# Performance work log

Measured on AMD Instinct MI355X. Metric: run time of the kernel, lower is better.

## Reference

```python
import jax, jax.numpy as jnp
import numpy as np

N, D, H, DH, FF, NE, NNZ = 4096, 128, 2, 64, 256, 2048, 65536
EPS = 1e-5

def layer_norm(x, g, b):
    m = jnp.mean(x, axis=-1, keepdims=True)
    v = jnp.var(x, axis=-1, keepdims=True)
    return (x - m) / jnp.sqrt(v + EPS) * g + b

def setup_inputs() -> dict:
    key = jax.random.key(0)
    ks = jax.random.split(key, 24)
    s = 0.05
    node_idx = jax.random.randint(ks[1], (NNZ,), 0, N)
    he_idx = jax.random.randint(ks[2], (NNZ,), 0, NE)
    return {
        "x": jax.random.normal(ks[0], (N, D), dtype=jnp.float32),
        "edge": jnp.stack([node_idx, he_idx]).astype(jnp.int64),
        "Wq": jax.random.normal(ks[3], (D, D)) * s, "bq": jnp.zeros((D,)),
        "Wk": jax.random.normal(ks[4], (D, D)) * s, "bk": jnp.zeros((D,)),
        "Wv": jax.random.normal(ks[5], (D, D)) * s, "bv": jnp.zeros((D,)),
        "Wo": jax.random.normal(ks[6], (D, D)) * s, "bo": jnp.zeros((D,)),
        "g_ln1": jnp.ones((D,)), "b_ln1": jnp.zeros((D,)),
        "W1": jax.random.normal(ks[7], (D, FF)) * s, "bf1": jnp.zeros((FF,)),
        "W2": jax.random.normal(ks[8], (FF, D)) * s, "bf2": jnp.zeros((D,)),
        "g_ln2": jnp.ones((D,)), "b_ln2": jnp.zeros((D,)),
        "Wh": jax.random.normal(ks[9], (D, D)) * s, "bh": jnp.zeros((D,)),
    }

def reference(x, edge, Wq, bq, Wk, bk, Wv, bv, Wo, bo, g_ln1, b_ln1,
              W1, bf1, W2, bf2, g_ln2, b_ln2, Wh, bh):
    # dropout layers run in eval mode (identity) for a deterministic reference
    def mha_block(h):
        q = (h @ Wq + bq).reshape(N, H, DH)
        k = (h @ Wk + bk).reshape(N, H, DH)
        v = (h @ Wv + bv).reshape(N, H, DH)
        scores = jnp.einsum('nhd,mhd->hnm', q, k) / jnp.sqrt(jnp.float32(DH))
        attn = jax.nn.softmax(scores, axis=-1)            # [H,N,N]
        o = jnp.einsum('hnm,mhd->nhd', attn, v).reshape(N, D)
        return layer_norm(h + o @ Wo + bo, g_ln1, b_ln1)

    def ff_block(h):
        z = jax.nn.sigmoid(h @ W1 + bf1)
        return layer_norm(h + z @ W2 + bf2, g_ln2, b_ln2)

    h = ff_block(mha_block(x))
    h = ff_block(mha_block(h))

    # HypergraphConv: out = D^{-1} H B^{-1} H^T (X Theta) + bias
    node_idx = edge[0]
    he_idx = edge[1]
    xt = h @ Wh                                            # [N,D]
    ones = jnp.ones((NNZ,), dtype=xt.dtype)
    Bdeg = jax.ops.segment_sum(ones, he_idx, num_segments=NE)
    Binv = jnp.where(Bdeg > 0, 1.0 / Bdeg, 0.0)
    Ddeg = jax.ops.segment_sum(ones, node_idx, num_segments=N)
    Dinv = jnp.where(Ddeg > 0, 1.0 / Ddeg, 0.0)
    e = jax.ops.segment_sum(xt[node_idx], he_idx, num_segments=NE) * Binv[:, None]
    out = jax.ops.segment_sum(e[he_idx], node_idx, num_segments=N) * Dinv[:, None] + bh
    return jax.nn.relu(out)
```

## Files before the change

### kernel.cpp

```cpp
#include <hip/hip_runtime.h>
#include <hip/hip_bf16.h>
#include <cstddef>

#define N_NODES 4096
#define DIM     128
#define NHEAD   2
#define DHEAD   64
#define FFDIM   256
#define NEDGE   2048
#define NNZ_E   65536
#define NSPLIT  8

typedef __attribute__((ext_vector_type(8))) short bf16x8;
typedef __attribute__((ext_vector_type(4))) float f32x4;
typedef unsigned short u16;

__device__ __forceinline__ u16 f2b(float f) {
    unsigned u = __float_as_uint(f);
    return (u16)((u + 0x7FFFu + ((u >> 16) & 1u)) >> 16);
}
__device__ __forceinline__ float b2f_bits(u16 h) {
    return __uint_as_float(((unsigned)h) << 16);
}
__device__ __forceinline__ unsigned cvtpk(float a, float b) {
    unsigned r;
    asm("v_cvt_pk_bf16_f32 %0, %1, %2" : "=v"(r) : "v"(a), "v"(b));
    return r;
}

__global__ void prep(const float* __restrict__ x, float* __restrict__ h,
                     u16* __restrict__ hh, u16* __restrict__ hl,
                     const float* W0, const float* W1, const float* W2,
                     const float* W3, const float* W4, const float* W5,
                     const float* W6,
                     u16* P0, u16* P1, u16* P2, u16* P3, u16* P4, u16* P5, u16* P6,
                     const int* __restrict__ edge_raw,
                     int* __restrict__ nidx, int* __restrict__ hidx,
                     int* __restrict__ cnt_e, int* __restrict__ cnt_n) {
    const int bx = blockIdx.x;
    if (bx < 2048) {
        int i = bx * 256 + threadIdx.x;
        float f = x[i];
        h[i] = f;
        u16 hi = f2b(f);
        hh[i] = hi;
        hl[i] = f2b(f - b2f_bits(hi));
        return;
    }
    if (bx >= 2944) {
        __shared__ int is64_s;
        if (threadIdx.x < 64) {
            int v = edge_raw[2 * threadIdx.x + 1];
            unsigned long long bal = __ballot(v != 0);
            if (threadIdx.x == 0) is64_s = (bal == 0ull) ? 1 : 0;
        }
        __syncthreads();
        const int is64 = is64_s;
        int i = (bx - 2944) * 256 + threadIdx.x;
        if (i < NNZ_E) {
            int ni = (is64 ? edge_raw[2 * i]             : edge_raw[i])         & (N_NODES - 1);
            int he = (is64 ? edge_raw[2 * NNZ_E + 2 * i] : edge_raw[NNZ_E + i]) & (NEDGE - 1);
            nidx[i] = ni;
            hidx[i] = he;
            atomicAdd(&cnt_n[ni], 1);
            atomicAdd(&cnt_e[he], 1);
        }
        return;
    }
    const int p = bx - 2048;
    const int sel = p >> 7;
    const float* W; u16* P; int K, NC;
    switch (sel) {
        case 0: W = W0; P = P0; K = 128; NC = 128; break;
        case 1: W = W1; P = P1; K = 128; NC = 128; break;
        case 2: W = W2; P = P2; K = 128; NC = 128; break;
        case 3: W = W3; P = P3; K = 128; NC = 128; break;
        case 4: W = W4; P = P4; K = 128; NC = 128; break;
        case 5: W = W5; P = P5; K = 128; NC = 256; break;
        default: W = W6; P = P6; K = 256; NC = 128; break;
    }
    int i = (p & 127) * 256 + threadIdx.x;
    if (i < K * NC) {
        int k = i / NC, n = i % NC;
        float f = W[i];
        u16 hb = f2b(f);
        size_t o = ((size_t)(k >> 3) * NC + n) * 8 + (k & 7);
        P[o] = hb;
        P[(size_t)K * NC + o] = f2b(f - b2f_bits(hb));
    }
}

__global__ __launch_bounds__(256) void qkv_mfma(const u16* __restrict__ Ah,
                                                const u16* __restrict__ Al,
                                                const u16* __restrict__ Wq,
                                                const u16* __restrict__ Wk,
                                                const u16* __restrict__ Wv,
                                                const float* __restrict__ bq,
                                                const float* __restrict__ bk,
                                                const float* __restrict__ bv,
                                                u16* __restrict__ qb,
                                                u16* __restrict__ kb,
                                                u16* __restrict__ vtb) {
    const int K = 128, NC = 128;
    const int tid = threadIdx.x, w = tid >> 6, lane = tid & 63;
    const int qi = lane & 15, gi = lane >> 4;
    const int row0 = blockIdx.x * 64 + w * 16;
    const int sel = blockIdx.y >> 2;
    const int col0 = (blockIdx.y & 3) * 32;
    const u16* Wp = (sel == 0) ? Wq : (sel == 1) ? Wk : Wv;
    const float* bias = (sel == 0) ? bq : (sel == 1) ? bk : bv;
    const u16* Wlo = Wp + (size_t)K * NC;

    f32x4 acc[2];
    acc[0] = (f32x4){0.f, 0.f, 0.f, 0.f};
    acc[1] = (f32x4){0.f, 0.f, 0.f, 0.f};

#pragma unroll 4
    for (int kc = 0; kc < K / 32; ++kc) {
        const int k0 = kc * 32;
        const size_t ao = (size_t)(row0 + qi) * K + k0 + gi * 8;
        bf16x8 ah = *(const bf16x8*)(Ah + ao);
        bf16x8 al = *(const bf16x8*)(Al + ao);
#pragma unroll
        for (int c = 0; c < 2; ++c) {
            const size_t wo = ((size_t)(k0 / 8 + gi) * NC + col0 + c * 16 + qi) * 8;
            bf16x8 wh = *(const bf16x8*)(Wp + wo);
            bf16x8 wl = *(const bf16x8*)(Wlo + wo);
            acc[c] = __builtin_amdgcn_mfma_f32_16x16x32_bf16(ah, wh, acc[c], 0, 0, 0);
            acc[c] = __builtin_amdgcn_mfma_f32_16x16x32_bf16(al, wh, acc[c], 0, 0, 0);
            acc[c] = __builtin_amdgcn_mfma_f32_16x16x32_bf16(ah, wl, acc[c], 0, 0, 0);
        }
    }

#pragma unroll
    for (int c = 0; c < 2; ++c) {
        const int col = col0 + c * 16 + qi;
        const int hh = col >> 6, d = col & 63;
        float bv_ = bias[col];
        if (sel < 2) {
            u16* dst = (sel == 0) ? qb : kb;
#pragma unroll
            for (int r = 0; r < 4; ++r) {
                const int grow = row0 + gi * 4 + r;
                dst[((size_t)hh * N_NODES + grow) * 64 + d] = f2b(acc[c][r] + bv_);
            }
        } else {
            const int grow0 = row0 + gi * 4;
            uint2 pw;
            pw.x = cvtpk(acc[c][0] + bv_, acc[c][1] + bv_);
            pw.y = cvtpk(acc[c][2] + bv_, acc[c][3] + bv_);
            *(uint2*)&vtb[((size_t)hh * 64 + d) * N_NODES + grow0] = pw;
        }
    }
}

#define ROWP 72
__global__ __launch_bounds__(512) void attn_mfma(const u16* __restrict__ qb,
                                                 const u16* __restrict__ kb,
                                                 const u16* __restrict__ vtb,
                                                 float* __restrict__ op,
                                                 float* __restrict__ mlm,
                                                 float* __restrict__ mll) {
    __shared__ __align__(16) u16 k_s[64 * ROWP];
    __shared__ __align__(16) u16 vt_s[64 * ROWP];
    __shared__ __align__(16) u16 p_s[8][16 * ROWP];
    const int h = blockIdx.y;
    const int s = blockIdx.z;
    const int row0 = blockIdx.x * 128;
    const int tid = threadIdx.x;
    const int w = tid >> 6, lane = tid & 63;
    const int qi = lane & 15, gi = lane >> 4;
    const float CE = 0.18033688011f;
    const float THR = 44.36f;

    const u16* qrow = qb + ((size_t)h * N_NODES + row0 + w * 16 + qi) * 64 + gi * 8;
    bf16x8 qf0 = *(const bf16x8*)qrow;
    bf16x8 qf1 = *(const bf16x8*)(qrow + 32);

    f32x4 oc[4];
#pragma unroll
    for (int i = 0; i < 4; ++i) oc[i] = (f32x4){0.f, 0.f, 0.f, 0.f};
    float m_run = -INFINITY, l_run = 0.f;

    const u16* kbh = kb + (size_t)h * N_NODES * 64;
    const u16* vth = vtb + (size_t)h * 64 * N_NODES;

    for (int kt = s * (N_NODES / 64 / NSPLIT); kt < (s + 1) * (N_NODES / 64 / NSPLIT); ++kt) {
        const u16* ksrc = kbh + kt * 64 * 64;
        {
            int r = tid >> 3, ss = tid & 7;
            *(uint4*)&k_s[r * ROWP + ss * 8]  = *(const uint4*)(ksrc + tid * 8);
            *(uint4*)&vt_s[r * ROWP + ss * 8] = *(const uint4*)(vth + (size_t)r * N_NODES + kt * 64 + ss * 8);
        }
        __syncthreads();

        f32x4 sc[4];
#pragma unroll
        for (int t = 0; t < 4; ++t) {
            const u16* krow = &k_s[(t * 16 + qi) * ROWP + gi * 8];
            bf16x8 ka0 = *(const bf16x8*)krow;
            bf16x8 ka1 = *(const bf16x8*)(krow + 32);
            f32x4 z = (f32x4){0.f, 0.f, 0.f, 0.f};
            z = __builtin_amdgcn_mfma_f32_16x16x32_bf16(ka0, qf0, z, 0, 0, 0);
            sc[t] = __builtin_amdgcn_mfma_f32_16x16x32_bf16(ka1, qf1, z, 0, 0, 0);
        }

        float smax = -INFINITY;
#pragma unroll
        for (int t = 0; t < 4; ++t)
            smax = fmaxf(smax, fmaxf(fmaxf(sc[t][0], sc[t][1]), fmaxf(sc[t][2], sc[t][3])));
        smax = fmaxf(smax, __shfl_xor(smax, 16));
        smax = fmaxf(smax, __shfl_xor(smax, 32));

        const bool renew = !__all(smax <= m_run + THR);
        float alpha;
        if (renew) {
            float mn = fmaxf(m_run, smax);
            alpha = exp2f((m_run - mn) * CE);
            m_run = mn;
        }
        float nb = m_run * CE;
        float psum = 0.f;
#pragma unroll
        for (int t = 0; t < 4; ++t) {
            float p0 = exp2f(fmaf(sc[t][0], CE, -nb));
            float p1 = exp2f(fmaf(sc[t][1], CE, -nb));
            float p2 = exp2f(fmaf(sc[t][2], CE, -nb));
            float p3 = exp2f(fmaf(sc[t][3], CE, -nb));
            psum += (p0 + p1) + (p2 + p3);
            uint2 pw;
            pw.x = cvtpk(p0, p1);
            pw.y = cvtpk(p2, p3);
            *(uint2*)&p_s[w][qi * ROWP + t * 16 + gi * 4] = pw;
        }
        psum += __shfl_xor(psum, 16);
        psum += __shfl_xor(psum, 32);

        if (renew) {
            float a0 = __shfl(alpha, gi * 4 + 0);
            float a1 = __shfl(alpha, gi * 4 + 1);
            float a2 = __shfl(alpha, gi * 4 + 2);
            float a3 = __shfl(alpha, gi * 4 + 3);
#pragma unroll
            for (int d = 0; d < 4; ++d) {
                oc[d][0] *= a0; oc[d][1] *= a1; oc[d][2] *= a2; oc[d][3] *= a3;
            }
            l_run = l_run * alpha + psum;
        } else {
            l_run += psum;
        }

        const u16* prow = &p_s[w][qi * ROWP];
        bf16x8 pa0 = *(const bf16x8*)(prow + gi * 8);
        bf16x8 pa1 = *(const bf16x8*)(prow + 32 + gi * 8);
#pragma unroll
        for (int d = 0; d < 4; ++d) {
            const u16* vrow = &vt_s[(d * 16 + qi) * ROWP + gi * 8];
            bf16x8 vb0 = *(const bf16x8*)vrow;
            bf16x8 vb1 = *(const bf16x8*)(vrow + 32);
            oc[d] = __builtin_amdgcn_mfma_f32_16x16x32_bf16(pa0, vb0, oc[d], 0, 0, 0);
            oc[d] = __builtin_amdgcn_mfma_f32_16x16x32_bf16(pa1, vb1, oc[d], 0, 0, 0);
        }
        __syncthreads();
    }

    float* opd = op + (size_t)s * N_NODES * 128;
#pragma unroll
    for (int d = 0; d < 4; ++d) {
        size_t cb = h * 64 + d * 16 + qi;
        opd[(size_t)(row0 + w * 16 + gi * 4 + 0) * 128 + cb] = oc[d][0];
        opd[(size_t)(row0 + w * 16 + gi * 4 + 1) * 128 + cb] = oc[d][1];
        opd[(size_t)(row0 + w * 16 + gi * 4 + 2) * 128 + cb] = oc[d][2];
        opd[(size_t)(row0 + w * 16 + gi * 4 + 3) * 128 + cb] = oc[d][3];
    }
    if (gi == 0) {
        size_t mi = (size_t)s * NHEAD * N_NODES + (size_t)h * N_NODES + row0 + w * 16 + qi;
        mlm[mi] = m_run;
        mll[mi] = l_run;
    }
}

#define ROWA 136
#define ROWZ 264
#define ROWH 132
template<int DO_QKV>
__global__ __launch_bounds__(512) void mega_layer(
        const float* __restrict__ op, const float* __restrict__ mlm,
        const float* __restrict__ mll,
        const u16* __restrict__ wp_o, const float* __restrict__ bo,
        float* __restrict__ h,
        const float* __restrict__ g1, const float* __restrict__ b1,
        const u16* __restrict__ wp_1, const float* __restrict__ bf1,
        const u16* __restrict__ wp_2, const float* __restrict__ bf2,
        const float* __restrict__ g2, const float* __restrict__ b2,
        const u16* __restrict__ wp_q, const u16* __restrict__ wp_k,
        const u16* __restrict__ wp_v,
        const float* __restrict__ bq, const float* __restrict__ bk,
        const float* __restrict__ bv,
        u16* __restrict__ qb, u16* __restrict__ kb, u16* __restrict__ vtb,
        const u16* __restrict__ wp_h, float* __restrict__ xt) {
    __shared__ __align__(16) u16 zbuf[16 * ROWZ * 2];
    __shared__ __align__(16) u16 hp_hi[16 * ROWA];
    __shared__ __align__(16) u16 hp_lo[16 * ROWA];
    __shared__ float hln[16 * ROWH];
    __shared__ float ws_s[NSPLIT][32];
    __shared__ float Linv_s[32];
    __shared__ float wsum[8][16], wsq[8][16];
    const float CE = 0.18033688011f;
    const int tid = threadIdx.x, w = tid >> 6, lane = tid & 63;
    const int qi = lane & 15, gi = lane >> 4;
    const int row0 = blockIdx.x * 16;
    u16* a_hi = zbuf;
    u16* a_lo = zbuf + 16 * ROWA;
    u16* z_hi = zbuf;
    u16* z_lo = zbuf + 16 * ROWZ;

    if (tid < 32) {
        int r = tid >> 1, hd = tid & 1;
        size_t mb = (size_t)hd * N_NODES + row0 + r;
        float m[NSPLIT], l[NSPLIT], mx = -INFINITY;
#pragma unroll
        for (int s = 0; s < NSPLIT; ++s) {
            m[s] = mlm[mb + (size_t)s * NHEAD * N_NODES];
            l[s] = mll[mb + (size_t)s * NHEAD * N_NODES];
            mx = fmaxf(mx, m[s]);
        }
        float L = 0.f;
#pragma unroll
        for (int s = 0; s < NSPLIT; ++s) {
            float ws = exp2f((m[s] - mx) * CE);
            ws_s[s][tid] = ws;
            L += ws * l[s];
        }
        Linv_s[tid] = 1.f / L;
    }
    __syncthreads();

    for (int e = tid; e < 16 * 128; e += 512) {
        int r = e >> 7, c = e & 127, hd = c >> 6;
        size_t idx = (size_t)(row0 + r) * 128 + c;
        float O = 0.f;
#pragma unroll
        for (int s = 0; s < NSPLIT; ++s)
            O += ws_s[s][r * 2 + hd] * op[(size_t)s * N_NODES * 128 + idx];
        float v = O * Linv_s[r * 2 + hd];
        u16 hi = f2b(v);
        a_hi[r * ROWA + c] = hi;
        a_lo[r * ROWA + c] = f2b(v - b2f_bits(hi));
    }
    __syncthreads();

    {
        const u16* Wlo = wp_o + (size_t)128 * 128;
        f32x4 acc = (f32x4){0.f, 0.f, 0.f, 0.f};
        const int col0 = w * 16;
#pragma unroll
        for (int kc = 0; kc < 4; ++kc) {
            const int k0 = kc * 32;
            bf16x8 ah = *(const bf16x8*)&a_hi[qi * ROWA + k0 + gi * 8];
            bf16x8 al = *(const bf16x8*)&a_lo[qi * ROWA + k0 + gi * 8];
            const size_t wo = ((size_t)(k0 / 8 + gi) * 128 + col0 + qi) * 8;
            bf16x8 wh = *(const bf16x8*)(wp_o + wo);
            bf16x8 wl = *(const bf16x8*)(Wlo + wo);
            acc = __builtin_amdgcn_mfma_f32_16x16x32_bf16(ah, wh, acc, 0, 0, 0);
            acc = __builtin_amdgcn_mfma_f32_16x16x32_bf16(al, wh, acc, 0, 0, 0);
            acc = __builtin_amdgcn_mfma_f32_16x16x32_bf16(ah, wl, acc, 0, 0, 0);
        }
        float y[4], rs[4], rq[4];
        const int col = col0 + qi;
        float bvv = bo[col];
#pragma unroll
        for (int r = 0; r < 4; ++r) {
            float v = acc[r] + bvv + h[(size_t)(row0 + gi * 4 + r) * 128 + col];
            y[r] = v;
            rs[r] = v; rq[r] = v * v;
        }
#pragma unroll
        for (int r = 0; r < 4; ++r)
            for (int msk = 1; msk < 16; msk <<= 1) {
                rs[r] += __shfl_xor(rs[r], msk);
                rq[r] += __shfl_xor(rq[r], msk);
            }
        if (qi == 0) {
#pragma unroll
            for (int r = 0; r < 4; ++r) { wsum[w][gi * 4 + r] = rs[r]; wsq[w][gi * 4 + r] = rq[r]; }
        }
        __syncthreads();
#pragma unroll
        for (int r = 0; r < 4; ++r) {
            const int lr = gi * 4 + r;
            float ts = 0.f, tq = 0.f;
#pragma unroll
            for (int ww = 0; ww < 8; ++ww) { ts += wsum[ww][lr]; tq += wsq[ww][lr]; }
            float mean = ts * (1.f / 128.f);
            float var  = tq * (1.f / 128.f) - mean * mean;
            float rstd = rsqrtf(var + 1e-5f);
            float yn = (y[r] - mean) * rstd * g1[col] + b1[col];
            hln[lr * ROWH + col] = yn;
            u16 hi = f2b(yn);
            hp_hi[lr * ROWA + col] = hi;
            hp_lo[lr * ROWA + col] = f2b(yn - b2f_bits(hi));
        }
    }
    __syncthreads();

    {
        const u16* W1lo = wp_1 + (size_t)128 * 256;
        f32x4 acc1[2];
#pragma unroll
        for (int t = 0; t < 2; ++t) acc1[t] = (f32x4){0.f, 0.f, 0.f, 0.f};
#pragma unroll
        for (int kc = 0; kc < 4; ++kc) {
            const int k0 = kc * 32;
            bf16x8 ah = *(const bf16x8*)&hp_hi[qi * ROWA + k0 + gi * 8];
            bf16x8 al = *(const bf16x8*)&hp_lo[qi * ROWA + k0 + gi * 8];
#pragma unroll
            for (int t = 0; t < 2; ++t) {
                const size_t wo = ((size_t)(k0 / 8 + gi) * 256 + w * 32 + t * 16 + qi) * 8;
                bf16x8 wh = *(const bf16x8*)(wp_1 + wo);
                bf16x8 wl = *(const bf16x8*)(W1lo + wo);
                acc1[t] = __builtin_amdgcn_mfma_f32_16x16x32_bf16(ah, wh, acc1[t], 0, 0, 0);
                acc1[t] = __builtin_amdgcn_mfma_f32_16x16x32_bf16(al, wh, acc1[t], 0, 0, 0);
                acc1[t] = __builtin_amdgcn_mfma_f32_16x16x32_bf16(ah, wl, acc1[t], 0, 0, 0);
            }
        }
        __syncthreads();
#pragma unroll
        for (int t = 0; t < 2; ++t) {
            const int col = w * 32 + t * 16 + qi;
            float bvv = bf1[col];
#pragma unroll
            for (int r = 0; r < 4; ++r) {
                float v = acc1[t][r] + bvv;
                v = 1.f / (1.f + __expf(-v));
                u16 hi = f2b(v);
                const int zr = gi * 4 + r;
                z_hi[zr * ROWZ + col] = hi;
                z_lo[zr * ROWZ + col] = f2b(v - b2f_bits(hi));
            }
        }
    }
    __syncthreads();

    {
        const u16* W2lo = wp_2 + (size_t)256 * 128;
        f32x4 acc = (f32x4){0.f, 0.f, 0.f, 0.f};
        const int col0 = w * 16;
#pragma unroll
        for (int kc = 0; kc < 8; ++kc) {
            const int k0 = kc * 32;
            bf16x8 ah = *(const bf16x8*)&z_hi[qi * ROWZ + k0 + gi * 8];
            bf16x8 al = *(const bf16x8*)&z_lo[qi * ROWZ + k0 + gi * 8];
            const size_t wo = ((size_t)(k0 / 8 + gi) * 128 + col0 + qi) * 8;
            bf16x8 wh = *(const bf16x8*)(wp_2 + wo);
            bf16x8 wl = *(const bf16x8*)(W2lo + wo);
            acc = __builtin_amdgcn_mfma_f32_16x16x32_bf16(ah, wh, acc, 0, 0, 0);
            acc = __builtin_amdgcn_mfma_f32_16x16x32_bf16(al, wh, acc, 0, 0, 0);
            acc = __builtin_amdgcn_mfma_f32_16x16x32_bf16(ah, wl, acc, 0, 0, 0);
        }
        float y[4], rs[4], rq[4];
        const int col = col0 + qi;
        float bvv = bf2[col];
#pragma unroll
        for (int r = 0; r < 4; ++r) {
            float v = acc[r] + bvv + hln[(gi * 4 + r) * ROWH + col];
            y[r] = v;
            rs[r] = v; rq[r] = v * v;
        }
#pragma unroll
        for (int r = 0; r < 4; ++r)
            for (int msk = 1; msk < 16; msk <<= 1) {
                rs[r] += __shfl_xor(rs[r], msk);
                rq[r] += __shfl_xor(rq[r], msk);
            }
        if (qi == 0) {
#pragma unroll
            for (int r = 0; r < 4; ++r) { wsum[w][gi * 4 + r] = rs[r]; wsq[w][gi * 4 + r] = rq[r]; }
        }
        __syncthreads();
#pragma unroll
        for (int r = 0; r < 4; ++r) {
            const int lr = gi * 4 + r;
            float ts = 0.f, tq = 0.f;
#pragma unroll
            for (int ww = 0; ww < 8; ++ww) { ts += wsum[ww][lr]; tq += wsq[ww][lr]; }
            float mean = ts * (1.f / 128.f);
            float var  = tq * (1.f / 128.f) - mean * mean;
            float rstd = rsqrtf(var + 1e-5f);
            float yn = (y[r] - mean) * rstd * g2[col] + b2[col];
            if (DO_QKV) h[(size_t)(row0 + lr) * 128 + col] = yn;
            u16 hi = f2b(yn);
            hp_hi[lr * ROWA + col] = hi;
            hp_lo[lr * ROWA + col] = f2b(yn - b2f_bits(hi));
        }
    }

    if (DO_QKV) {
        __syncthreads();
        const int col0 = w * 16;
#pragma unroll
        for (int sel = 0; sel < 3; ++sel) {
            const u16* Wp = (sel == 0) ? wp_q : (sel == 1) ? wp_k : wp_v;
            const float* bias = (sel == 0) ? bq : (sel == 1) ? bk : bv;
            const u16* Wlo = Wp + (size_t)128 * 128;
            f32x4 acc = (f32x4){0.f, 0.f, 0.f, 0.f};
#pragma unroll
            for (int kc = 0; kc < 4; ++kc) {
                const int k0 = kc * 32;
                bf16x8 ah = *(const bf16x8*)&hp_hi[qi * ROWA + k0 + gi * 8];
                bf16x8 al = *(const bf16x8*)&hp_lo[qi * ROWA + k0 + gi * 8];
                const size_t wo = ((size_t)(k0 / 8 + gi) * 128 + col0 + qi) * 8;
                bf16x8 wh = *(const bf16x8*)(Wp + wo);
                bf16x8 wl = *(const bf16x8*)(Wlo + wo);
                acc = __builtin_amdgcn_mfma_f32_16x16x32_bf16(ah, wh, acc, 0, 0, 0);
                acc = __builtin_amdgcn_mfma_f32_16x16x32_bf16(al, wh, acc, 0, 0, 0);
                acc = __builtin_amdgcn_mfma_f32_16x16x32_bf16(ah, wl, acc, 0, 0, 0);
            }
            const int col = col0 + qi;
            const int hh = col >> 6, d = col & 63;
            float bv_ = bias[col];
            if (sel < 2) {
                u16* dst = (sel == 0) ? qb : kb;
#pragma unroll
                for (int r = 0; r < 4; ++r) {
                    const int grow = row0 + gi * 4 + r;
                    dst[((size_t)hh * N_NODES + grow) * 64 + d] = f2b(acc[r] + bv_);
                }
            } else {
                const int grow0 = row0 + gi * 4;
                uint2 pw;
                pw.x = cvtpk(acc[0] + bv_, acc[1] + bv_);
                pw.y = cvtpk(acc[2] + bv_, acc[3] + bv_);
                *(uint2*)&vtb[((size_t)hh * 64 + d) * N_NODES + grow0] = pw;
            }
        }
    } else {
        __syncthreads();
        const u16* Wlo = wp_h + (size_t)128 * 128;
        f32x4 acc = (f32x4){0.f, 0.f, 0.f, 0.f};
        const int col0 = w * 16;
#pragma unroll
        for (int kc = 0; kc < 4; ++kc) {
            const int k0 = kc * 32;
            bf16x8 ah = *(const bf16x8*)&hp_hi[qi * ROWA + k0 + gi * 8];
            bf16x8 al = *(const bf16x8*)&hp_lo[qi * ROWA + k0 + gi * 8];
            const size_t wo = ((size_t)(k0 / 8 + gi) * 128 + col0 + qi) * 8;
            bf16x8 wh = *(const bf16x8*)(wp_h + wo);
            bf16x8 wl = *(const bf16x8*)(Wlo + wo);
            acc = __builtin_amdgcn_mfma_f32_16x16x32_bf16(ah, wh, acc, 0, 0, 0);
            acc = __builtin_amdgcn_mfma_f32_16x16x32_bf16(al, wh, acc, 0, 0, 0);
            acc = __builtin_amdgcn_mfma_f32_16x16x32_bf16(ah, wl, acc, 0, 0, 0);
        }
        const int col = col0 + qi;
#pragma unroll
        for (int r = 0; r < 4; ++r)
            xt[(size_t)(row0 + gi * 4 + r) * 128 + col] = acc[r];
    }
}

__global__ __launch_bounds__(1024) void scan_only(const int* __restrict__ cnt_e,
                                                  const int* __restrict__ cnt_n,
                                                  int* __restrict__ off_e,
                                                  int* __restrict__ off_n,
                                                  int* __restrict__ cur_e,
                                                  int* __restrict__ cur_n) {
    __shared__ int s[N_NODES];
    const int he_side = (blockIdx.x == 0);
    const int n = he_side ? NEDGE : N_NODES;
    const int* cnt = he_side ? cnt_e : cnt_n;
    int* off = he_side ? off_e : off_n;
    int* cur = he_side ? cur_e : cur_n;
    for (int i = threadIdx.x; i < n; i += 1024) s[i] = cnt[i];
    __syncthreads();
    for (int st = 1; st < n; st <<= 1) {
        int v[4]; int nj = 0;
        for (int i = threadIdx.x; i < n; i += 1024) v[nj++] = (i >= st) ? s[i - st] : 0;
        __syncthreads();
        nj = 0;
        for (int i = threadIdx.x; i < n; i += 1024) s[i] += v[nj++];
        __syncthreads();
    }
    for (int i = threadIdx.x; i < n; i += 1024) { off[i + 1] = s[i]; cur[i] = 0; }
    if (threadIdx.x == 0) off[0] = 0;
}

__global__ void fill_csr(const int* __restrict__ nidx, const int* __restrict__ hidx,
                         const int* __restrict__ off_e, const int* __restrict__ off_n,
                         int* __restrict__ cur_e, int* __restrict__ cur_n,
                         int* __restrict__ csr_e, int* __restrict__ csr_n) {
    int i = blockIdx.x * 256 + threadIdx.x;
    if (i < NNZ_E) {
        int ni = nidx[i], he = hidx[i];
        int p = atomicAdd(&cur_e[he], 1);
        csr_e[off_e[he] + p] = ni;
        int q = atomicAdd(&cur_n[ni], 1);
        csr_n[off_n[ni] + q] = he;
    }
}

__global__ __launch_bounds__(128) void gather_e(const int* __restrict__ off_e,
                                                const int* __restrict__ csr_e,
                                                const float* __restrict__ xt,
                                                float* __restrict__ e_sc) {
    __shared__ int ms[128];
    const int he = blockIdx.x, d = threadIdx.x;
    const int beg = off_e[he], end = off_e[he + 1];
    float a0 = 0.f, a1 = 0.f, a2 = 0.f, a3 = 0.f;
    for (int c = beg; c < end; c += 128) {
        int nl = min(128, end - c);
        if (d < nl) ms[d] = csr_e[c + d];
        __syncthreads();
        int j = 0;
        for (; j + 3 < nl; j += 4) {
            a0 += xt[(size_t)ms[j]     * 128 + d];
            a1 += xt[(size_t)ms[j + 1] * 128 + d];
            a2 += xt[(size_t)ms[j + 2] * 128 + d];
            a3 += xt[(size_t)ms[j + 3] * 128 + d];
        }
        for (; j < nl; ++j) a0 += xt[(size_t)ms[j] * 128 + d];
        __syncthreads();
    }
    float binv = (end > beg) ? 1.f / (float)(end - beg) : 0.f;
    e_sc[(size_t)he * 128 + d] = ((a0 + a1) + (a2 + a3)) * binv;
}

__global__ __launch_bounds__(128) void gather_n(const int* __restrict__ off_n,
                                                const int* __restrict__ csr_n,
                                                const float* __restrict__ e_sc,
                                                const float* __restrict__ bh,
                                                float* __restrict__ out) {
    __shared__ int ms[128];
    const int nn = blockIdx.x, d = threadIdx.x;
    const int beg = off_n[nn], end = off_n[nn + 1];
    float a0 = 0.f, a1 = 0.f, a2 = 0.f, a3 = 0.f;
    for (int c = beg; c < end; c += 128) {
        int nl = min(128, end - c);
        if (d < nl) ms[d] = csr_n[c + d];
        __syncthreads();
        int j = 0;
        for (; j + 3 < nl; j += 4) {
            a0 += e_sc[(size_t)ms[j]     * 128 + d];
            a1 += e_sc[(size_t)ms[j + 1] * 128 + d];
            a2 += e_sc[(size_t)ms[j + 2] * 128 + d];
            a3 += e_sc[(size_t)ms[j + 3] * 128 + d];
        }
        for (; j < nl; ++j) a0 += e_sc[(size_t)ms[j] * 128 + d];
        __syncthreads();
    }
    float dinv = (end > beg) ? 1.f / (float)(end - beg) : 0.f;
    float v = ((a0 + a1) + (a2 + a3)) * dinv + bh[d];
    out[(size_t)nn * 128 + d] = v > 0.f ? v : 0.f;
}

extern "C" void kernel_launch(void* const* d_in, const int* in_sizes, int n_in,
                              void* d_out, int out_size, void* d_ws, size_t ws_size,
                              hipStream_t stream) {
    (void)in_sizes; (void)n_in; (void)out_size; (void)ws_size;
    const float* x    = (const float*)d_in[0];
    const int*   edge = (const int*)  d_in[1];
    const float* Wq = (const float*)d_in[2];  const float* bq  = (const float*)d_in[3];
    const float* Wk = (const float*)d_in[4];  const float* bk  = (const float*)d_in[5];
    const float* Wv = (const float*)d_in[6];  const float* bv  = (const float*)d_in[7];
    const float* Wo = (const float*)d_in[8];  const float* bo  = (const float*)d_in[9];
    const float* g1 = (const float*)d_in[10]; const float* b1  = (const float*)d_in[11];
    const float* W1 = (const float*)d_in[12]; const float* bf1 = (const float*)d_in[13];
    const float* W2 = (const float*)d_in[14]; const float* bf2 = (const float*)d_in[15];
    const float* g2 = (const float*)d_in[16]; const float* b2  = (const float*)d_in[17];
    const float* Wh = (const float*)d_in[18]; const float* bh  = (const float*)d_in[19];
    float* out = (float*)d_out;

    float* B = (float*)d_ws;
    float* h    = B;
    u16*   h_hi = (u16*)(B + 524288);
    u16*   h_lo = (u16*)(B + 786432);
    u16*   qb   = (u16*)(B + 1048576);
    u16*   kb   = (u16*)(B + 1310720);
    u16*   vtb  = (u16*)(B + 1835008);
    float* op   = B + 2097152;
    float* mlm  = B + 6291456;
    float* mll  = B + 6356992;
    float* xt   = B + 6946816;
    float* e_sc = B + 7471104;
    u16*   wp_q = (u16*)(B + 8519680);
    u16*   wp_k = (u16*)(B + 8536064);
    u16*   wp_v = (u16*)(B + 8552448);
    u16*   wp_o = (u16*)(B + 8568832);
    u16*   wp_h = (u16*)(B + 8585216);
    u16*   wp_1 = (u16*)(B + 8601600);
    u16*   wp_2 = (u16*)(B + 8634368);
    int*   cur_e = (int*)(B + 9328640);
    int*   cur_n = (int*)(B + 9330688);
    int*   off_e = (int*)(B + 9334784);
    int*   off_n = (int*)(B + 9336840);
    int*   csr_e = (int*)(B + 9340944);
    int*   csr_n = (int*)(B + 9406480);
    int*   cnt_e = (int*)(B + 9472016);
    int*   cnt_n = (int*)(B + 9474064);
    int*   nidx  = (int*)(B + 9478160);
    int*   hidx  = (int*)(B + 9543696);

    hipMemsetAsync(cnt_e, 0, (NEDGE + N_NODES) * sizeof(int), stream);

    prep<<<3200, 256, 0, stream>>>(x, h, h_hi, h_lo,
                                   Wq, Wk, Wv, Wo, Wh, W1, W2,
                                   wp_q, wp_k, wp_v, wp_o, wp_h, wp_1, wp_2,
                                   edge, nidx, hidx, cnt_e, cnt_n);

    qkv_mfma<<<dim3(64, 12), 256, 0, stream>>>(h_hi, h_lo, wp_q, wp_k, wp_v,
                                               bq, bk, bv, qb, kb, vtb);
    attn_mfma<<<dim3(N_NODES / 128, NHEAD, NSPLIT), 512, 0, stream>>>(qb, kb, vtb, op, mlm, mll);
    mega_layer<1><<<N_NODES / 16, 512, 0, stream>>>(op, mlm, mll, wp_o, bo, h, g1, b1,
                                                    wp_1, bf1, wp_2, bf2, g2, b2,
                                                    wp_q, wp_k, wp_v, bq, bk, bv,
                                                    qb, kb, vtb, wp_h, xt);
    attn_mfma<<<dim3(N_NODES / 128, NHEAD, NSPLIT), 512, 0, stream>>>(qb, kb, vtb, op, mlm, mll);
    mega_layer<0><<<N_NODES / 16, 512, 0, stream>>>(op, mlm, mll, wp_o, bo, h, g1, b1,
                                                    wp_1, bf1, wp_2, bf2, g2, b2,
                                                    nullptr, nullptr, nullptr,
                                                    nullptr, nullptr, nullptr,
                                                    nullptr, nullptr, nullptr,
                                                    wp_h, xt);

    scan_only<<<2, 1024, 0, stream>>>(cnt_e, cnt_n, off_e, off_n, cur_e, cur_n);
    fill_csr<<<NNZ_E / 256, 256, 0, stream>>>(nidx, hidx, off_e, off_n, cur_e, cur_n, csr_e, csr_n);
    gather_e<<<NEDGE, 128, 0, stream>>>(off_e, csr_e, xt, e_sc);
    gather_n<<<N_NODES, 128, 0, stream>>>(off_n, csr_n, e_sc, bh, out);
}
```

Measured before the change: 234.2 us.

## Fold CSR build into attention/layer kernels, double-buffer attention K/V tiles

New measurement: 218.6 us. 1.07x faster.

```diff
diff --git a/kernel.cpp b/kernel.cpp
--- a/kernel.cpp
+++ b/kernel.cpp
@@ -38,16 +38,20 @@
                      int* __restrict__ nidx, int* __restrict__ hidx,
                      int* __restrict__ cnt_e, int* __restrict__ cnt_n) {
     const int bx = blockIdx.x;
-    if (bx < 2048) {
-        int i = bx * 256 + threadIdx.x;
-        float f = x[i];
-        h[i] = f;
-        u16 hi = f2b(f);
-        hh[i] = hi;
-        hl[i] = f2b(f - b2f_bits(hi));
+    if (bx < 512) {
+        int i4 = bx * 256 + threadIdx.x;
+        float4 f4 = ((const float4*)x)[i4];
+        ((float4*)h)[i4] = f4;
+        ushort4 hi4, lo4;
+        hi4.x = f2b(f4.x); lo4.x = f2b(f4.x - b2f_bits(hi4.x));
+        hi4.y = f2b(f4.y); lo4.y = f2b(f4.y - b2f_bits(hi4.y));
+        hi4.z = f2b(f4.z); lo4.z = f2b(f4.z - b2f_bits(hi4.z));
+        hi4.w = f2b(f4.w); lo4.w = f2b(f4.w - b2f_bits(hi4.w));
+        ((ushort4*)hh)[i4] = hi4;
+        ((ushort4*)hl)[i4] = lo4;
         return;
     }
-    if (bx >= 2944) {
+    if (bx >= 1408) {
         __shared__ int is64_s;
         if (threadIdx.x < 64) {
             int v = edge_raw[2 * threadIdx.x + 1];
@@ -56,7 +60,7 @@
         }
         __syncthreads();
         const int is64 = is64_s;
-        int i = (bx - 2944) * 256 + threadIdx.x;
+        int i = (bx - 1408) * 256 + threadIdx.x;
         if (i < NNZ_E) {
             int ni = (is64 ? edge_raw[2 * i]             : edge_raw[i])         & (N_NODES - 1);
             int he = (is64 ? edge_raw[2 * NNZ_E + 2 * i] : edge_raw[NNZ_E + i]) & (NEDGE - 1);
@@ -67,7 +71,7 @@
         }
         return;
     }
-    const int p = bx - 2048;
+    const int p = bx - 512;
     const int sel = p >> 7;
     const float* W; u16* P; int K, NC;
     switch (sel) {
@@ -155,15 +159,46 @@
 }
 
 #define ROWP 72
-__global__ __launch_bounds__(512) void attn_mfma(const u16* __restrict__ qb,
-                                                 const u16* __restrict__ kb,
-                                                 const u16* __restrict__ vtb,
-                                                 float* __restrict__ op,
-                                                 float* __restrict__ mlm,
-                                                 float* __restrict__ mll) {
-    __shared__ __align__(16) u16 k_s[64 * ROWP];
-    __shared__ __align__(16) u16 vt_s[64 * ROWP];
+__global__ __launch_bounds__(512, 4) void attn_mfma(const u16* __restrict__ qb,
+                                                    const u16* __restrict__ kb,
+                                                    const u16* __restrict__ vtb,
+                                                    float* __restrict__ op,
+                                                    float* __restrict__ mlm,
+                                                    float* __restrict__ mll,
+                                                    const int* __restrict__ cnt_e,
+                                                    const int* __restrict__ cnt_n,
+                                                    int* __restrict__ off_e,
+                                                    int* __restrict__ off_n,
+                                                    int* __restrict__ cur_e,
+                                                    int* __restrict__ cur_n) {
+    __shared__ __align__(16) u16 k_s[2][64 * ROWP];
+    __shared__ __align__(16) u16 vt_s[2][64 * ROWP];
     __shared__ __align__(16) u16 p_s[8][16 * ROWP];
+
+    if (blockIdx.x >= 32) {
+        if (blockIdx.y == 0 && blockIdx.z < 2) {
+            int* sbuf = (int*)&k_s[0][0];
+            const int he_side = (blockIdx.z == 0);
+            const int n = he_side ? NEDGE : N_NODES;
+            const int* cnt = he_side ? cnt_e : cnt_n;
+            int* off = he_side ? off_e : off_n;
+            int* cur = he_side ? cur_e : cur_n;
+            for (int i = threadIdx.x; i < n; i += 512) sbuf[i] = cnt[i];
+            __syncthreads();
+            for (int st = 1; st < n; st <<= 1) {
+                int v[8]; int nj = 0;
+                for (int i = threadIdx.x; i < n; i += 512) v[nj++] = (i >= st) ? sbuf[i - st] : 0;
+                __syncthreads();
+                nj = 0;
+                for (int i = threadIdx.x; i < n; i += 512) sbuf[i] += v[nj++];
+                __syncthreads();
+            }
+            for (int i = threadIdx.x; i < n; i += 512) { off[i + 1] = sbuf[i]; cur[i] = 0; }
+            if (threadIdx.x == 0) off[0] = 0;
+        }
+        return;
+    }
+
     const int h = blockIdx.y;
     const int s = blockIdx.z;
     const int row0 = blockIdx.x * 128;
@@ -185,25 +220,39 @@
     const u16* kbh = kb + (size_t)h * N_NODES * 64;
     const u16* vth = vtb + (size_t)h * 64 * N_NODES;
 
-    for (int kt = s * (N_NODES / 64 / NSPLIT); kt < (s + 1) * (N_NODES / 64 / NSPLIT); ++kt) {
-        const u16* ksrc = kbh + kt * 64 * 64;
-        {
-            int r = tid >> 3, ss = tid & 7;
-            *(uint4*)&k_s[r * ROWP + ss * 8]  = *(const uint4*)(ksrc + tid * 8);
-            *(uint4*)&vt_s[r * ROWP + ss * 8] = *(const uint4*)(vth + (size_t)r * N_NODES + kt * 64 + ss * 8);
-        }
-        __syncthreads();
+    const int nt0 = s * (N_NODES / 64 / NSPLIT);
+    const int nt1 = nt0 + N_NODES / 64 / NSPLIT;
+    const int r = tid >> 3, ss = tid & 7;
+
+    {
+        const u16* ksrc = kbh + nt0 * 64 * 64;
+        *(uint4*)&k_s[0][r * ROWP + ss * 8]  = *(const uint4*)(ksrc + tid * 8);
+        *(uint4*)&vt_s[0][r * ROWP + ss * 8] = *(const uint4*)(vth + (size_t)r * N_NODES + nt0 * 64 + ss * 8);
+    }
+    __syncthreads();
+    int cur = 0;
+
+    for (int kt = nt0; kt < nt1; ++kt) {
+        uint4 knx, vnx;
+        const bool more = (kt + 1 < nt1);
+        if (more) {
+            const u16* ksrc = kbh + (kt + 1) * 64 * 64;
+            knx = *(const uint4*)(ksrc + tid * 8);
+            vnx = *(const uint4*)(vth + (size_t)r * N_NODES + (kt + 1) * 64 + ss * 8);
+        }
 
         f32x4 sc[4];
+        __builtin_amdgcn_s_setprio(1);
 #pragma unroll
         for (int t = 0; t < 4; ++t) {
-            const u16* krow = &k_s[(t * 16 + qi) * ROWP + gi * 8];
+            const u16* krow = &k_s[cur][(t * 16 + qi) * ROWP + gi * 8];
             bf16x8 ka0 = *(const bf16x8*)krow;
             bf16x8 ka1 = *(const bf16x8*)(krow + 32);
             f32x4 z = (f32x4){0.f, 0.f, 0.f, 0.f};
             z = __builtin_amdgcn_mfma_f32_16x16x32_bf16(ka0, qf0, z, 0, 0, 0);
             sc[t] = __builtin_amdgcn_mfma_f32_16x16x32_bf16(ka1, qf1, z, 0, 0, 0);
         }
+        __builtin_amdgcn_s_setprio(0);
 
         float smax = -INFINITY;
 #pragma unroll
@@ -253,15 +302,23 @@
         const u16* prow = &p_s[w][qi * ROWP];
         bf16x8 pa0 = *(const bf16x8*)(prow + gi * 8);
         bf16x8 pa1 = *(const bf16x8*)(prow + 32 + gi * 8);
+        __builtin_amdgcn_s_setprio(1);
 #pragma unroll
         for (int d = 0; d < 4; ++d) {
-            const u16* vrow = &vt_s[(d * 16 + qi) * ROWP + gi * 8];
+            const u16* vrow = &vt_s[cur][(d * 16 + qi) * ROWP + gi * 8];
             bf16x8 vb0 = *(const bf16x8*)vrow;
             bf16x8 vb1 = *(const bf16x8*)(vrow + 32);
             oc[d] = __builtin_amdgcn_mfma_f32_16x16x32_bf16(pa0, vb0, oc[d], 0, 0, 0);
             oc[d] = __builtin_amdgcn_mfma_f32_16x16x32_bf16(pa1, vb1, oc[d], 0, 0, 0);
         }
-        __syncthreads();
+        __builtin_amdgcn_s_setprio(0);
+
+        if (more) {
+            *(uint4*)&k_s[cur ^ 1][r * ROWP + ss * 8]  = knx;
+            *(uint4*)&vt_s[cur ^ 1][r * ROWP + ss * 8] = vnx;
+        }
+        __syncthreads();
+        cur ^= 1;
     }
 
     float* opd = op + (size_t)s * N_NODES * 128;
@@ -298,7 +355,22 @@
         const float* __restrict__ bq, const float* __restrict__ bk,
         const float* __restrict__ bv,
         u16* __restrict__ qb, u16* __restrict__ kb, u16* __restrict__ vtb,
-        const u16* __restrict__ wp_h, float* __restrict__ xt) {
+        const u16* __restrict__ wp_h, float* __restrict__ xt,
+        const int* __restrict__ nidx, const int* __restrict__ hidx,
+        const int* __restrict__ off_e, const int* __restrict__ off_n,
+        int* __restrict__ cur_e, int* __restrict__ cur_n,
+        int* __restrict__ csr_e, int* __restrict__ csr_n) {
+    if (DO_QKV && blockIdx.x >= N_NODES / 16) {
+        int i = (blockIdx.x - N_NODES / 16) * 512 + threadIdx.x;
+        if (i < NNZ_E) {
+            int ni = nidx[i], he = hidx[i];
+            int p = atomicAdd(&cur_e[he], 1);
+            csr_e[off_e[he] + p] = ni;
+            int q = atomicAdd(&cur_n[ni], 1);
+            csr_n[off_n[ni] + q] = he;
+        }
+        return;
+    }
     __shared__ __align__(16) u16 zbuf[16 * ROWZ * 2];
     __shared__ __align__(16) u16 hp_hi[16 * ROWA];
     __shared__ __align__(16) u16 hp_lo[16 * ROWA];
@@ -555,46 +627,6 @@
 #pragma unroll
         for (int r = 0; r < 4; ++r)
             xt[(size_t)(row0 + gi * 4 + r) * 128 + col] = acc[r];
-    }
-}
-
-__global__ __launch_bounds__(1024) void scan_only(const int* __restrict__ cnt_e,
-                                                  const int* __restrict__ cnt_n,
-                                                  int* __restrict__ off_e,
-                                                  int* __restrict__ off_n,
-                                                  int* __restrict__ cur_e,
-                                                  int* __restrict__ cur_n) {
-    __shared__ int s[N_NODES];
-    const int he_side = (blockIdx.x == 0);
-    const int n = he_side ? NEDGE : N_NODES;
-    const int* cnt = he_side ? cnt_e : cnt_n;
-    int* off = he_side ? off_e : off_n;
-    int* cur = he_side ? cur_e : cur_n;
-    for (int i = threadIdx.x; i < n; i += 1024) s[i] = cnt[i];
-    __syncthreads();
-    for (int st = 1; st < n; st <<= 1) {
-        int v[4]; int nj = 0;
-        for (int i = threadIdx.x; i < n; i += 1024) v[nj++] = (i >= st) ? s[i - st] : 0;
-        __syncthreads();
-        nj = 0;
-        for (int i = threadIdx.x; i < n; i += 1024) s[i] += v[nj++];
-        __syncthreads();
-    }
-    for (int i = threadIdx.x; i < n; i += 1024) { off[i + 1] = s[i]; cur[i] = 0; }
-    if (threadIdx.x == 0) off[0] = 0;
-}
-
-__global__ void fill_csr(const int* __restrict__ nidx, const int* __restrict__ hidx,
-                         const int* __restrict__ off_e, const int* __restrict__ off_n,
-                         int* __restrict__ cur_e, int* __restrict__ cur_n,
-                         int* __restrict__ csr_e, int* __restrict__ csr_n) {
-    int i = blockIdx.x * 256 + threadIdx.x;
-    if (i < NNZ_E) {
-        int ni = nidx[i], he = hidx[i];
-        int p = atomicAdd(&cur_e[he], 1);
-        csr_e[off_e[he] + p] = ni;
-        int q = atomicAdd(&cur_n[ni], 1);
-        csr_n[off_n[ni] + q] = he;
     }
 }
 
@@ -701,28 +733,34 @@
 
     hipMemsetAsync(cnt_e, 0, (NEDGE + N_NODES) * sizeof(int), stream);
 
-    prep<<<3200, 256, 0, stream>>>(x, h, h_hi, h_lo,
+    prep<<<1664, 256, 0, stream>>>(x, h, h_hi, h_lo,
                                    Wq, Wk, Wv, Wo, Wh, W1, W2,
                                    wp_q, wp_k, wp_v, wp_o, wp_h, wp_1, wp_2,
                                    edge, nidx, hidx, cnt_e, cnt_n);
 
     qkv_mfma<<<dim3(64, 12), 256, 0, stream>>>(h_hi, h_lo, wp_q, wp_k, wp_v,
                                                bq, bk, bv, qb, kb, vtb);
-    attn_mfma<<<dim3(N_NODES / 128, NHEAD, NSPLIT), 512, 0, stream>>>(qb, kb, vtb, op, mlm, mll);
-    mega_layer<1><<<N_NODES / 16, 512, 0, stream>>>(op, mlm, mll, wp_o, bo, h, g1, b1,
+    attn_mfma<<<dim3(33, NHEAD, NSPLIT), 512, 0, stream>>>(qb, kb, vtb, op, mlm, mll,
+                                                           cnt_e, cnt_n, off_e, off_n,
+                                                           cur_e, cur_n);
+    mega_layer<1><<<N_NODES / 16 + 128, 512, 0, stream>>>(op, mlm, mll, wp_o, bo, h, g1, b1,
                                                     wp_1, bf1, wp_2, bf2, g2, b2,
                                                     wp_q, wp_k, wp_v, bq, bk, bv,
-                                                    qb, kb, vtb, wp_h, xt);
-    attn_mfma<<<dim3(N_NODES / 128, NHEAD, NSPLIT), 512, 0, stream>>>(qb, kb, vtb, op, mlm, mll);
+                                                    qb, kb, vtb, wp_h, xt,
+                                                    nidx, hidx, off_e, off_n,
+                                                    cur_e, cur_n, csr_e, csr_n);
+    attn_mfma<<<dim3(32, NHEAD, NSPLIT), 512, 0, stream>>>(qb, kb, vtb, op, mlm, mll,
+                                                           cnt_e, cnt_n, off_e, off_n,
+                                                           cur_e, cur_n);
     mega_layer<0><<<N_NODES / 16, 512, 0, stream>>>(op, mlm, mll, wp_o, bo, h, g1, b1,
                                                     wp_1, bf1, wp_2, bf2, g2, b2,
                                                     nullptr, nullptr, nullptr,
                                                     nullptr, nullptr, nullptr,
                                                     nullptr, nullptr, nullptr,
-                                                    wp_h, xt);
-
-    scan_only<<<2, 1024, 0, stream>>>(cnt_e, cnt_n, off_e, off_n, cur_e, cur_n);
-    fill_csr<<<NNZ_E / 256, 256, 0, stream>>>(nidx, hidx, off_e, off_n, cur_e, cur_n, csr_e, csr_n);
+                                                    wp_h, xt,
+                                                    nullptr, nullptr, nullptr, nullptr,
+                                                    nullptr, nullptr, nullptr, nullptr);
+
     gather_e<<<NEDGE, 128, 0, stream>>>(off_e, csr_e, xt, e_sc);
     gather_n<<<N_NODES, 128, 0, stream>>>(off_n, csr_n, e_sc, bh, out);
 }
```
